# Kernel optimization log

Hardware: AMD Instinct MI355X
Metric: run time of the kernel (lower is better)

The kernel has to match this reference:

```python
import jax, jax.numpy as jnp
import numpy as np

N_HEAD = 12

def setup_inputs() -> dict:
    key = jax.random.key(0)
    ks = jax.random.split(key, 3)
    B, T, D = 4, 2048, 768
    x = jax.random.normal(ks[0], (B, T, D), dtype=jnp.float32)
    W_qkv = jax.random.normal(ks[1], (D, 3 * D), dtype=jnp.float32) * (1.0 / np.sqrt(D))
    b_qkv = jnp.zeros((3 * D,), dtype=jnp.float32)
    W_o = jax.random.normal(ks[2], (D, D), dtype=jnp.float32) * (1.0 / np.sqrt(D))
    b_o = jnp.zeros((D,), dtype=jnp.float32)
    return {"x": x, "W_qkv": W_qkv, "b_qkv": b_qkv, "W_o": W_o, "b_o": b_o}


def reference(x, W_qkv, b_qkv, W_o, b_o):
    B, T, D = x.shape
    H = N_HEAD
    hd = D // H
    qkv = x @ W_qkv + b_qkv                      # [B,T,3D]
    q, k, v = jnp.split(qkv, 3, axis=-1)
    # [B,T,D] -> [B,H,T,hd]
    q = q.reshape(B, T, H, hd).transpose(0, 2, 1, 3)
    k = k.reshape(B, T, H, hd).transpose(0, 2, 1, 3)
    v = v.reshape(B, T, H, hd).transpose(0, 2, 1, 3)
    scale = 1.0 / np.sqrt(hd).astype(np.float32)
    scores = jnp.einsum('bhqd,bhkd->bhqk', q, k) * scale   # [B,H,T,T]
    causal = jnp.tril(jnp.ones((T, T), dtype=bool))
    scores = jnp.where(causal[None, None, :, :], scores, -jnp.inf)
    attn = jax.nn.softmax(scores, axis=-1)
    out = jnp.einsum('bhqk,bhkd->bhqd', attn, v)            # [B,H,T,hd]
    out = out.transpose(0, 2, 1, 3).reshape(B, T, D)
    return out @ W_o + b_o
```

## Files before the change

### kernel.cpp

```cpp
#include <hip/hip_runtime.h>
#include <hip/hip_bf16.h>

typedef __bf16 bf16_t;
typedef float f32x4 __attribute__((ext_vector_type(4)));
typedef bf16_t bf16x8 __attribute__((ext_vector_type(8)));
typedef bf16_t bf16x4 __attribute__((ext_vector_type(4)));

#define MFMA16(a, b, c) __builtin_amdgcn_mfma_f32_16x16x32_bf16(a, b, c, 0, 0, 0)

#define QSCALE 0.18033688011112042f

__device__ __forceinline__ void gl_lds16(const bf16_t* g, bf16_t* l) {
    __builtin_amdgcn_global_load_lds(
        (const __attribute__((address_space(1))) unsigned int*)g,
        (__attribute__((address_space(3))) unsigned int*)l, 16, 0, 0);
}

__global__ __launch_bounds__(256) void conv_x(const float* __restrict__ in,
                                              bf16_t* __restrict__ out, int n) {
    int i = (blockIdx.x * 256 + threadIdx.x) * 4;
    if (i >= n) return;
    float4 v = *(const float4*)(in + i);
    bf16x4 o = { (bf16_t)v.x, (bf16_t)v.y, (bf16_t)v.z, (bf16_t)v.w };
    *(bf16x4*)(out + i) = o;
}

__global__ __launch_bounds__(256) void conv_t(const float* __restrict__ in,
                                              bf16_t* __restrict__ out,
                                              int R, int C) {
    __shared__ float t[32][33];
    const int bx = blockIdx.x * 32;
    const int by = blockIdx.y * 32;
    const int tx = threadIdx.x & 31;
    const int ty = threadIdx.x >> 5;
#pragma unroll
    for (int i = 0; i < 4; i++)
        t[ty + i * 8][tx] = in[(size_t)(by + ty + i * 8) * C + bx + tx];
    __syncthreads();
#pragma unroll
    for (int i = 0; i < 4; i++)
        out[(size_t)(bx + ty + i * 8) * R + by + tx] = (bf16_t)t[tx][ty + i * 8];
}

template <int EPI>
__global__ __launch_bounds__(256) void gemm_bt(
    const bf16_t* __restrict__ A, const bf16_t* __restrict__ Bt,
    const float* __restrict__ bias,
    void* __restrict__ O0v, bf16_t* __restrict__ O1, bf16_t* __restrict__ O2,
    int M, int N, int K)
{
    __shared__ __align__(16) bf16_t As[2][128 * 32];
    __shared__ __align__(16) bf16_t Bs[2][128 * 32];

    const int tid  = threadIdx.x;
    const int wid  = tid >> 6;
    const int lane = tid & 63;
    const int quad = lane >> 4;
    const int l15  = lane & 15;
    const int wm   = (wid >> 1) * 64;
    const int wn   = (wid & 1) * 64;

    const int mtiles = M >> 7;
    const int mtpx   = mtiles >> 3;
    const int bid    = blockIdx.x;
    const int xcd    = bid & 7;
    const int slot   = bid >> 3;
    const int m0     = (xcd * mtpx + (slot % mtpx)) << 7;
    const int n0     = (slot / mtpx) << 7;

    f32x4 acc[4][4];
#pragma unroll
    for (int i = 0; i < 4; i++)
#pragma unroll
        for (int j = 0; j < 4; j++) acc[i][j] = (f32x4){0.f, 0.f, 0.f, 0.f};

    const int srow = tid >> 2;
    const int scol = (tid & 3) * 8;
    const bf16_t* ag0 = A  + (size_t)(m0 + srow) * K + scol;
    const bf16_t* ag1 = A  + (size_t)(m0 + 64 + srow) * K + scol;
    const bf16_t* bg0 = Bt + (size_t)(n0 + srow) * K + scol;
    const bf16_t* bg1 = Bt + (size_t)(n0 + 64 + srow) * K + scol;

    auto prefetch = [&](int k0, int buf) {
        gl_lds16(ag0 + k0, As[buf] + tid * 8);
        gl_lds16(ag1 + k0, As[buf] + 2048 + tid * 8);
        gl_lds16(bg0 + k0, Bs[buf] + tid * 8);
        gl_lds16(bg1 + k0, Bs[buf] + 2048 + tid * 8);
    };

    const int niter = K >> 5;
    prefetch(0, 0);
    for (int i = 0; i < niter; i++) {
        __syncthreads();
        if (i + 1 < niter) prefetch((i + 1) << 5, (i + 1) & 1);
        const bf16_t* Ap = As[i & 1];
        const bf16_t* Bp = Bs[i & 1];

        bf16x8 af[4], bfr[4];
#pragma unroll
        for (int ii = 0; ii < 4; ii++)
            af[ii] = *(const bf16x8*)(Ap + (wm + ii * 16 + l15) * 32 + quad * 8);
#pragma unroll
        for (int j = 0; j < 4; j++)
            bfr[j] = *(const bf16x8*)(Bp + (wn + j * 16 + l15) * 32 + quad * 8);
#pragma unroll
        for (int ii = 0; ii < 4; ii++)
#pragma unroll
            for (int j = 0; j < 4; j++)
                acc[ii][j] = MFMA16(af[ii], bfr[j], acc[ii][j]);
        __syncthreads();
    }

#pragma unroll
    for (int i = 0; i < 4; i++) {
        const int mbase = m0 + wm + i * 16 + quad * 4;
#pragma unroll
        for (int j = 0; j < 4; j++) {
            const int n  = n0 + wn + j * 16 + l15;
            const float bv = bias[n];
#pragma unroll
            for (int r = 0; r < 4; r++) {
                const float c = acc[i][j][r] + bv;
                const int mm  = mbase + r;
                if (EPI == 0) {
                    const int sec  = n / 768;
                    const int d    = n - sec * 768;
                    const int h    = d >> 6;
                    const int feat = d & 63;
                    const int b    = mm >> 11;
                    const int tt   = mm & 2047;
                    const int bh   = b * 12 + h;
                    if (sec == 0)
                        ((bf16_t*)O0v)[(((size_t)bh * 2048 + tt) << 6) + feat] = (bf16_t)(c * QSCALE);
                    else if (sec == 1)
                        O1[(((size_t)bh * 2048 + tt) << 6) + feat] = (bf16_t)c;
                    else
                        O2[(((size_t)bh * 64 + feat) << 11) + tt] = (bf16_t)c;
                } else {
                    ((float*)O0v)[(size_t)mm * N + n] = c;
                }
            }
        }
    }
}

__global__ __launch_bounds__(256) void attn_k(
    const bf16_t* __restrict__ Q, const bf16_t* __restrict__ Kb,
    const bf16_t* __restrict__ Vt,
    bf16_t* __restrict__ Op0, bf16_t* __restrict__ Op1,
    float* __restrict__ Lp0, float* __restrict__ Lp1)
{
    constexpr int LDSP = 72;
    __shared__ __align__(16) bf16_t Ks[2 * 4096];
    __shared__ __align__(16) bf16_t Vs[2 * 4096];
    __shared__ __align__(16) bf16_t Ps[4 * 16 * LDSP];

    const int tid  = threadIdx.x;
    const int wid  = tid >> 6;
    const int lane = tid & 63;
    const int quad = lane >> 4;
    const int l15  = lane & 15;

    const int bid  = blockIdx.x;
    const int xcd  = bid & 7;
    const int slot = bid >> 3;
    const int bh   = xcd * 6 + (slot >> 5);
    const int px   = slot & 31;
    const int p    = px >> 1;
    const int hpar = px & 1;

    const bf16_t* Qb  = Q  + ((size_t)bh << 17);
    const bf16_t* Kbh = Kb + ((size_t)bh << 17);
    const bf16_t* Vbh = Vt + ((size_t)bh << 17);

    bf16_t* Pw = Ps + wid * 16 * LDSP;
    bf16_t* Op = hpar ? Op1 : Op0;
    float*  Lp = hpar ? Lp1 : Lp0;

    const bf16x8 ones = { (bf16_t)1.f, (bf16_t)1.f, (bf16_t)1.f, (bf16_t)1.f,
                          (bf16_t)1.f, (bf16_t)1.f, (bf16_t)1.f, (bf16_t)1.f };

    const int srow = tid >> 2;
    const int scol = (tid & 3) * 8;

    auto prefetch = [&](int j, int buf) {
        const int kv0 = j * 64;
        bf16_t* kd = Ks + buf * 4096 + tid * 8;
        bf16_t* vd = Vs + buf * 4096 + tid * 8;
#pragma unroll
        for (int c = 0; c < 2; c++) {
            gl_lds16(Kbh + (size_t)(kv0 + srow) * 64 + c * 32 + scol, kd + c * 2048);
            gl_lds16(Vbh + (size_t)srow * 2048 + kv0 + c * 32 + scol, vd + c * 2048);
        }
    };

#pragma unroll
    for (int half = 0; half < 2; half++) {
        const int qt = half == 0 ? (31 - p) : p;
        const int q0 = qt * 64;

        bf16x8 qf[2];
        {
            const bf16_t* qp = Qb + ((size_t)(q0 + wid * 16 + l15) << 6) + quad * 8;
            qf[0] = *(const bf16x8*)(qp);
            qf[1] = *(const bf16x8*)(qp + 32);
        }

        f32x4 lacc = (f32x4){0.f, 0.f, 0.f, 0.f};
        f32x4 oacc[4];
#pragma unroll
        for (int f = 0; f < 4; f++) oacc[f] = (f32x4){0.f, 0.f, 0.f, 0.f};

        const int cnt = (qt >= hpar) ? ((qt - hpar) >> 1) + 1 : 0;
        if (cnt > 0) prefetch(hpar, 0);

        for (int i = 0; i < cnt; i++) {
            const int j   = hpar + 2 * i;
            const int kv0 = j * 64;
            __syncthreads();
            if (i + 1 < cnt) prefetch(j + 2, (i + 1) & 1);
            const bf16_t* Kp = Ks + (i & 1) * 4096;
            const bf16_t* Vp = Vs + (i & 1) * 4096;

            f32x4 s[4];
#pragma unroll
            for (int c = 0; c < 4; c++) {
                s[c] = (f32x4){0.f, 0.f, 0.f, 0.f};
#pragma unroll
                for (int kk = 0; kk < 2; kk++) {
                    bf16x8 kf = *(const bf16x8*)(Kp + kk * 2048 + (c * 16 + l15) * 32 + quad * 8);
                    s[c] = MFMA16(qf[kk], kf, s[c]);
                }
            }

            if (j == qt) {
                const int qrow_base = q0 + wid * 16 + quad * 4;
#pragma unroll
                for (int c = 0; c < 4; c++) {
                    const int kvg = kv0 + c * 16 + l15;
#pragma unroll
                    for (int r = 0; r < 4; r++)
                        if (kvg > qrow_base + r) s[c][r] = -3e38f;
                }
            }

#pragma unroll
            for (int c = 0; c < 4; c++)
#pragma unroll
                for (int r = 0; r < 4; r++)
                    Pw[(quad * 4 + r) * LDSP + c * 16 + l15] = (bf16_t)exp2f(s[c][r]);

            bf16x8 pa[2];
#pragma unroll
            for (int kk = 0; kk < 2; kk++)
                pa[kk] = *(const bf16x8*)(Pw + l15 * LDSP + kk * 32 + quad * 8);

            lacc = MFMA16(pa[0], ones, lacc);
            lacc = MFMA16(pa[1], ones, lacc);

#pragma unroll
            for (int f = 0; f < 4; f++)
#pragma unroll
                for (int kk = 0; kk < 2; kk++) {
                    bf16x8 vf = *(const bf16x8*)(Vp + kk * 2048 + (f * 16 + l15) * 32 + quad * 8);
                    oacc[f] = MFMA16(pa[kk], vf, oacc[f]);
                }
        }
        __syncthreads();

        const int trow = q0 + wid * 16 + quad * 4;
#pragma unroll
        for (int r = 0; r < 4; r++) {
#pragma unroll
            for (int f = 0; f < 4; f++)
                Op[(((size_t)bh * 2048 + trow + r) << 6) + f * 16 + l15] =
                    (bf16_t)oacc[f][r];
        }
        if (l15 == 0) {
#pragma unroll
            for (int r = 0; r < 4; r++)
                Lp[(size_t)bh * 2048 + trow + r] = lacc[r];
        }
    }
}

__global__ __launch_bounds__(256) void comb_k(
    const bf16_t* __restrict__ Op0, const bf16_t* __restrict__ Op1,
    const float* __restrict__ Lp0, const float* __restrict__ Lp1,
    bf16_t* __restrict__ AO)
{
    const size_t e  = ((size_t)blockIdx.x * 256 + threadIdx.x) * 8;
    const int bh    = (int)(e >> 17);
    const int t     = (int)(e >> 6) & 2047;
    const int feat  = (int)e & 63;
    const int b     = bh / 12;
    const int h     = bh - b * 12;
    const float inv = 1.0f / (Lp0[(size_t)bh * 2048 + t] + Lp1[(size_t)bh * 2048 + t]);
    bf16x8 o0 = *(const bf16x8*)(Op0 + e);
    bf16x8 o1 = *(const bf16x8*)(Op1 + e);
    bf16x8 o;
#pragma unroll
    for (int k = 0; k < 8; k++)
        o[k] = (bf16_t)(((float)o0[k] + (float)o1[k]) * inv);
    *(bf16x8*)(AO + ((size_t)(b * 2048 + t) * 768 + h * 64 + feat)) = o;
}

extern "C" void kernel_launch(void* const* d_in, const int* in_sizes, int n_in,
                              void* d_out, int out_size, void* d_ws, size_t ws_size,
                              hipStream_t stream)
{
    const float* x    = (const float*)d_in[0];
    const float* Wqkv = (const float*)d_in[1];
    const float* bqkv = (const float*)d_in[2];
    const float* Wo   = (const float*)d_in[3];
    const float* bo   = (const float*)d_in[4];
    float* out = (float*)d_out;

    const size_t per = (size_t)48 * 2048 * 64;
    bf16_t* Qs  = (bf16_t*)d_ws;
    bf16_t* Kk  = Qs + per;
    bf16_t* Vt  = Kk + per;
    bf16_t* AO  = Vt + per;
    bf16_t* xb  = AO + per;
    bf16_t* Wt  = xb + per;
    bf16_t* Wot = Wt + (size_t)2304 * 768;
    float*  Lp0 = (float*)(Wot + (size_t)768 * 768);
    float*  Lp1 = Lp0 + (size_t)48 * 2048;
    bf16_t* Op0 = xb;
    bf16_t* Op1 = (bf16_t*)d_out;

    conv_x<<<6144, 256, 0, stream>>>(x, xb, 8192 * 768);
    conv_t<<<dim3(72, 24), 256, 0, stream>>>(Wqkv, Wt, 768, 2304);
    conv_t<<<dim3(24, 24), 256, 0, stream>>>(Wo, Wot, 768, 768);

    gemm_bt<0><<<18 * 64, 256, 0, stream>>>(
        xb, Wt, bqkv, (void*)Qs, Kk, Vt, 8192, 2304, 768);
    attn_k<<<1536, 256, 0, stream>>>(Qs, Kk, Vt, Op0, Op1, Lp0, Lp1);
    comb_k<<<3072, 256, 0, stream>>>(Op0, Op1, Lp0, Lp1, AO);
    gemm_bt<1><<<6 * 64, 256, 0, stream>>>(
        AO, Wot, bo, (void*)out, nullptr, nullptr, 8192, 768, 768);
}
```

Measured before the change: 235.8 us.

## Transpose attention MFMA operands, swizzle P tile in LDS, vectorize output stores

Swaps the MFMA operand order so scores come out transposed (kv along rows per lane). Each lane can then write packed bf16x4 P values into an XOR-swizzled, unpadded LDS tile and store outputs as bf16x4 vectors instead of scalar bf16. It also replaces exp2f with a raw v_exp_f32 instruction. The aim is to cut LDS bank conflicts, the number of scalar stores, and exp overhead. The cost is more complex indexing, plus an unused inverse computation.

```diff
diff --git a/kernel.cpp b/kernel.cpp
--- a/kernel.cpp
+++ b/kernel.cpp
@@ -14,6 +14,12 @@
     __builtin_amdgcn_global_load_lds(
         (const __attribute__((address_space(1))) unsigned int*)g,
         (__attribute__((address_space(3))) unsigned int*)l, 16, 0, 0);
+}
+
+__device__ __forceinline__ float fexp2(float x) {
+    float y;
+    asm("v_exp_f32 %0, %1" : "=v"(y) : "v"(x));
+    return y;
 }
 
 __global__ __launch_bounds__(256) void conv_x(const float* __restrict__ in,
@@ -150,10 +156,9 @@
     bf16_t* __restrict__ Op0, bf16_t* __restrict__ Op1,
     float* __restrict__ Lp0, float* __restrict__ Lp1)
 {
-    constexpr int LDSP = 72;
     __shared__ __align__(16) bf16_t Ks[2 * 4096];
     __shared__ __align__(16) bf16_t Vs[2 * 4096];
-    __shared__ __align__(16) bf16_t Ps[4 * 16 * LDSP];
+    __shared__ __align__(16) bf16_t Ps[4 * 16 * 64];
 
     const int tid  = threadIdx.x;
     const int wid  = tid >> 6;
@@ -173,7 +178,17 @@
     const bf16_t* Kbh = Kb + ((size_t)bh << 17);
     const bf16_t* Vbh = Vt + ((size_t)bh << 17);
 
-    bf16_t* Pw = Ps + wid * 16 * LDSP;
+    bf16_t* Pw = Ps + wid * 1024;
+    const int swl = l15 & 7;
+    bf16_t* pwr[4];
+#pragma unroll
+    for (int c = 0; c < 4; c++)
+        pwr[c] = Pw + l15 * 64 + (((((c << 1) | (quad >> 1))) ^ swl) << 3) + ((quad & 1) << 2);
+    const bf16_t* prd[2];
+#pragma unroll
+    for (int kk = 0; kk < 2; kk++)
+        prd[kk] = Pw + l15 * 64 + ((((kk << 2) | quad) ^ swl) << 3);
+
     bf16_t* Op = hpar ? Op1 : Op0;
     float*  Lp = hpar ? Lp1 : Lp0;
 
@@ -198,10 +213,11 @@
     for (int half = 0; half < 2; half++) {
         const int qt = half == 0 ? (31 - p) : p;
         const int q0 = qt * 64;
+        const int qg = q0 + wid * 16 + l15;
 
         bf16x8 qf[2];
         {
-            const bf16_t* qp = Qb + ((size_t)(q0 + wid * 16 + l15) << 6) + quad * 8;
+            const bf16_t* qp = Qb + ((size_t)qg << 6) + quad * 8;
             qf[0] = *(const bf16x8*)(qp);
             qf[1] = *(const bf16x8*)(qp + 32);
         }
@@ -222,65 +238,61 @@
             const bf16_t* Kp = Ks + (i & 1) * 4096;
             const bf16_t* Vp = Vs + (i & 1) * 4096;
 
-            f32x4 s[4];
+            f32x4 st[4];
 #pragma unroll
             for (int c = 0; c < 4; c++) {
-                s[c] = (f32x4){0.f, 0.f, 0.f, 0.f};
+                st[c] = (f32x4){0.f, 0.f, 0.f, 0.f};
 #pragma unroll
                 for (int kk = 0; kk < 2; kk++) {
                     bf16x8 kf = *(const bf16x8*)(Kp + kk * 2048 + (c * 16 + l15) * 32 + quad * 8);
-                    s[c] = MFMA16(qf[kk], kf, s[c]);
+                    st[c] = MFMA16(kf, qf[kk], st[c]);
                 }
             }
 
             if (j == qt) {
-                const int qrow_base = q0 + wid * 16 + quad * 4;
-#pragma unroll
-                for (int c = 0; c < 4; c++) {
-                    const int kvg = kv0 + c * 16 + l15;
+                const int kvb = kv0 + quad * 4;
+#pragma unroll
+                for (int c = 0; c < 4; c++)
 #pragma unroll
                     for (int r = 0; r < 4; r++)
-                        if (kvg > qrow_base + r) s[c][r] = -3e38f;
-                }
+                        if (kvb + c * 16 + r > qg) st[c][r] = -3e38f;
             }
 
 #pragma unroll
-            for (int c = 0; c < 4; c++)
-#pragma unroll
-                for (int r = 0; r < 4; r++)
-                    Pw[(quad * 4 + r) * LDSP + c * 16 + l15] = (bf16_t)exp2f(s[c][r]);
-
-            bf16x8 pa[2];
+            for (int c = 0; c < 4; c++) {
+                bf16x4 pk = { (bf16_t)fexp2(st[c][0]), (bf16_t)fexp2(st[c][1]),
+                              (bf16_t)fexp2(st[c][2]), (bf16_t)fexp2(st[c][3]) };
+                *(bf16x4*)pwr[c] = pk;
+            }
+
+            bf16x8 pb[2];
 #pragma unroll
             for (int kk = 0; kk < 2; kk++)
-                pa[kk] = *(const bf16x8*)(Pw + l15 * LDSP + kk * 32 + quad * 8);
-
-            lacc = MFMA16(pa[0], ones, lacc);
-            lacc = MFMA16(pa[1], ones, lacc);
+                pb[kk] = *(const bf16x8*)prd[kk];
+
+            lacc = MFMA16(ones, pb[0], lacc);
+            lacc = MFMA16(ones, pb[1], lacc);
 
 #pragma unroll
             for (int f = 0; f < 4; f++)
 #pragma unroll
                 for (int kk = 0; kk < 2; kk++) {
                     bf16x8 vf = *(const bf16x8*)(Vp + kk * 2048 + (f * 16 + l15) * 32 + quad * 8);
-                    oacc[f] = MFMA16(pa[kk], vf, oacc[f]);
+                    oacc[f] = MFMA16(vf, pb[kk], oacc[f]);
                 }
         }
         __syncthreads();
 
-        const int trow = q0 + wid * 16 + quad * 4;
-#pragma unroll
-        for (int r = 0; r < 4; r++) {
-#pragma unroll
-            for (int f = 0; f < 4; f++)
-                Op[(((size_t)bh * 2048 + trow + r) << 6) + f * 16 + l15] =
-                    (bf16_t)oacc[f][r];
-        }
-        if (l15 == 0) {
-#pragma unroll
-            for (int r = 0; r < 4; r++)
-                Lp[(size_t)bh * 2048 + trow + r] = lacc[r];
-        }
+        const float inv = (lacc[0] > 0.f) ? 1.0f / lacc[0] : 0.f;
+        const size_t obase = (((size_t)bh * 2048 + qg) << 6) + quad * 4;
+#pragma unroll
+        for (int f = 0; f < 4; f++) {
+            bf16x4 o = { (bf16_t)(oacc[f][0]), (bf16_t)(oacc[f][1]),
+                         (bf16_t)(oacc[f][2]), (bf16_t)(oacc[f][3]) };
+            *(bf16x4*)(Op + obase + f * 16) = o;
+        }
+        (void)inv;
+        if (quad == 0) Lp[(size_t)bh * 2048 + qg] = lacc[0];
     }
 }
 
```

After: 224.2 us. 4.9% less time.
